# Kernel optimization log

Measured on AMD Instinct MI355X. Metric: run time of the kernel, lower is better.

Reference implementation:

```python
import jax, jax.numpy as jnp
import numpy as np

B, S, D, H = 2, 2048, 1024, 16
HD = D // H  # head dim = 64


def setup_inputs() -> dict:
    key = jax.random.key(0)
    ks = jax.random.split(key, 5)
    scale = 1.0 / np.sqrt(D)
    return {
        "hidden_states": jax.random.normal(ks[0], (B, S, D), jnp.float32),
        "attention_mask": jax.random.normal(ks[1], (B, 1, 1, S), jnp.float32),
        "Wq": jax.random.normal(ks[2], (D, D), jnp.float32) * scale,
        "bq": jnp.zeros((D,), jnp.float32),
        "Wk": jax.random.normal(ks[3], (D, D), jnp.float32) * scale,
        "bk": jnp.zeros((D,), jnp.float32),
        "Wv": jax.random.normal(ks[4], (D, D), jnp.float32) * scale,
        "bv": jnp.zeros((D,), jnp.float32),
    }


def _split_heads(x):
    # [B,S,D] -> [B,H,S,HD]
    return x.reshape(B, S, H, HD).transpose(0, 2, 1, 3)


def reference(hidden_states, attention_mask, Wq, bq, Wk, bk, Wv, bv):
    # torch Linear: y = x @ W.T + b
    q = _split_heads(hidden_states @ Wq.T + bq)
    k = _split_heads(hidden_states @ Wk.T + bk)
    v = _split_heads(hidden_states @ Wv.T + bv)

    scores = jnp.einsum("bhqd,bhkd->bhqk", q, k)
    # Faithful to source: with a mask present, the 1/sqrt(head_dim) scaling
    # is overwritten and raw scores are multiplied by the binary key mask.
    mask = (attention_mask >= 0).astype(scores.dtype)  # [B,1,1,S]
    probs = scores * mask
    # dropout prob = 0 (eval) -> identity

    ctx = jnp.einsum("bhqk,bhkd->bhqd", probs, v)
    ctx = ctx.transpose(0, 2, 1, 3).reshape(B, S, D)
    return ctx
```

## Files before the change

### kernel.cpp

```cpp
#include <hip/hip_runtime.h>

#define BB 2
#define SS 2048
#define DD 1024
#define HH 16
#define HDIM 64
#define MTOT 4096

typedef unsigned short u16;
typedef __bf16 bf16_t;
typedef bf16_t bf16x8 __attribute__((ext_vector_type(8)));
typedef float floatx4 __attribute__((ext_vector_type(4)));
typedef float floatx16 __attribute__((ext_vector_type(16)));

__device__ __forceinline__ float bf2f(u16 u) {
  union { unsigned int i; float f; } x;
  x.i = ((unsigned int)u) << 16;
  return x.f;
}
__device__ __forceinline__ u16 f2bf(float f) {
  union { float f; unsigned int i; } x;
  x.f = f;
  unsigned int r = x.i + 0x7fffu + ((x.i >> 16) & 1u);
  return (u16)(r >> 16);
}

__device__ __forceinline__ void gload16(const u16* g, u16* l) {
  __builtin_amdgcn_global_load_lds(
      (const __attribute__((address_space(1))) unsigned int*)g,
      (__attribute__((address_space(3))) unsigned int*)l, 16, 0, 0);
}

__global__ __launch_bounds__(256) void cast_to_bf16(
    const float* __restrict__ hs, const float* __restrict__ wq,
    const float* __restrict__ wk, const float* __restrict__ wv,
    u16* __restrict__ hs_b, u16* __restrict__ wq_b,
    u16* __restrict__ wk_b, u16* __restrict__ wv_b) {
  int fid = blockIdx.x * 256 + threadIdx.x;
  const float* src;
  u16* dst;
  int local;
  if (fid < 1048576) { src = hs; dst = hs_b; local = fid; }
  else if (fid < 1310720) { src = wq; dst = wq_b; local = fid - 1048576; }
  else if (fid < 1572864) { src = wk; dst = wk_b; local = fid - 1310720; }
  else { src = wv; dst = wv_b; local = fid - 1572864; }
  float4 v = reinterpret_cast<const float4*>(src)[local];
  ushort4 o;
  o.x = f2bf(v.x); o.y = f2bf(v.y); o.z = f2bf(v.z); o.w = f2bf(v.w);
  reinterpret_cast<ushort4*>(dst)[local] = o;
}

#define BKK 32
__global__ __launch_bounds__(256) void qkv_gemm_kernel(
    const u16* __restrict__ A,
    const u16* __restrict__ Wq, const u16* __restrict__ Wk, const u16* __restrict__ Wv,
    const float* __restrict__ bq, const float* __restrict__ bk, const float* __restrict__ bv,
    u16* __restrict__ Qo, u16* __restrict__ Ko, u16* __restrict__ Vo) {
  __shared__ u16 sA[128 * BKK];
  __shared__ u16 sB[128 * BKK];
  const int mt = blockIdx.y, ntall = blockIdx.x;
  const int seg = ntall >> 3, nt = ntall & 7;
  const u16* Wp = (seg == 0) ? Wq : (seg == 1) ? Wk : Wv;
  const float* bp = (seg == 0) ? bq : (seg == 1) ? bk : bv;
  u16* Out = (seg == 0) ? Qo : (seg == 1) ? Ko : Vo;
  const int m0 = mt * 128, n0 = nt * 128;
  const int tid = threadIdx.x;
  const int lane = tid & 63, wave = tid >> 6;
  const int wm = (wave >> 1) * 64, wn = (wave & 1) * 64;
  const int l32 = lane & 31, khalf = lane >> 5;
  const int srow0 = wave * 32 + (lane >> 2);
  const int scol = (lane & 3) * 8;
  floatx16 acc[2][2] = {};
  for (int k0 = 0; k0 < DD; k0 += BKK) {
#pragma unroll
    for (int c = 0; c < 2; ++c) {
      int r = srow0 + c * 16;
      gload16(A + (size_t)(m0 + r) * DD + k0 + scol, sA + r * BKK + scol);
      gload16(Wp + (size_t)(n0 + r) * DD + k0 + scol, sB + r * BKK + scol);
    }
    __syncthreads();
#pragma unroll
    for (int kk = 0; kk < 2; ++kk) {
      bf16x8 af[2], bfr[2];
#pragma unroll
      for (int i = 0; i < 2; ++i)
        af[i] = *reinterpret_cast<const bf16x8*>(sA + (wm + i * 32 + l32) * BKK + kk * 16 + khalf * 8);
#pragma unroll
      for (int j = 0; j < 2; ++j)
        bfr[j] = *reinterpret_cast<const bf16x8*>(sB + (wn + j * 32 + l32) * BKK + kk * 16 + khalf * 8);
#pragma unroll
      for (int i = 0; i < 2; ++i)
#pragma unroll
        for (int j = 0; j < 2; ++j)
          acc[i][j] = __builtin_amdgcn_mfma_f32_32x32x16_bf16(af[i], bfr[j], acc[i][j], 0, 0, 0);
    }
    __syncthreads();
  }
#pragma unroll
  for (int j = 0; j < 2; ++j) {
    int col = n0 + wn + j * 32 + l32;
    float bias = bp[col];
#pragma unroll
    for (int i = 0; i < 2; ++i) {
#pragma unroll
      for (int reg = 0; reg < 16; ++reg) {
        int row = m0 + wm + i * 32 + (reg & 3) + 8 * (reg >> 2) + 4 * khalf;
        Out[(size_t)row * DD + col] = f2bf(acc[i][j][reg] + bias);
      }
    }
  }
}

__global__ __launch_bounds__(256) void m_partial_kernel(
    const u16* __restrict__ Kb, const u16* __restrict__ Vb,
    const float* __restrict__ am, float* __restrict__ mpart) {
  __shared__ float sK[64 * 68];
  __shared__ float sV[64 * 68];
  const int bh = blockIdx.y;
  const int b = bh >> 4, h = bh & 15;
  const int tid = threadIdx.x;
  const int e0 = (tid & 15) * 4, d0 = (tid >> 4) * 4;
  float acc[4][4] = {};
  for (int cs = 0; cs < 4; ++cs) {
    const int s0 = (blockIdx.x * 4 + cs) * 64;
    if (cs) __syncthreads();
#pragma unroll
    for (int c = 0; c < 2; ++c) {
      int L = tid + c * 256;
      int srow = L >> 3;
      int col = (L & 7) * 8;
      size_t g = (size_t)(b * SS + s0 + srow) * DD + h * HDIM + col;
      uint4 kraw = *reinterpret_cast<const uint4*>(Kb + g);
      uint4 vraw = *reinterpret_cast<const uint4*>(Vb + g);
      float m = (am[b * SS + s0 + srow] >= 0.f) ? 1.f : 0.f;
      unsigned int kw[4] = {kraw.x, kraw.y, kraw.z, kraw.w};
      unsigned int vw[4] = {vraw.x, vraw.y, vraw.z, vraw.w};
#pragma unroll
      for (int q = 0; q < 4; ++q) {
        sK[srow * 68 + col + 2 * q]     = m * bf2f((u16)(kw[q] & 0xffffu));
        sK[srow * 68 + col + 2 * q + 1] = m * bf2f((u16)(kw[q] >> 16));
        sV[srow * 68 + col + 2 * q]     = bf2f((u16)(vw[q] & 0xffffu));
        sV[srow * 68 + col + 2 * q + 1] = bf2f((u16)(vw[q] >> 16));
      }
    }
    __syncthreads();
    for (int s = 0; s < 64; ++s) {
      float4 kk = *reinterpret_cast<const float4*>(&sK[s * 68 + e0]);
      float4 vv = *reinterpret_cast<const float4*>(&sV[s * 68 + d0]);
      float ka[4] = {kk.x, kk.y, kk.z, kk.w};
      float va[4] = {vv.x, vv.y, vv.z, vv.w};
#pragma unroll
      for (int i = 0; i < 4; ++i)
#pragma unroll
        for (int j = 0; j < 4; ++j) acc[i][j] += ka[i] * va[j];
    }
  }
  float* outp = mpart + ((size_t)(blockIdx.x * 32 + bh)) * 4096;
#pragma unroll
  for (int i = 0; i < 4; ++i) {
    float4 o = {acc[i][0], acc[i][1], acc[i][2], acc[i][3]};
    *reinterpret_cast<float4*>(&outp[(e0 + i) * 64 + d0]) = o;
  }
}

__global__ __launch_bounds__(256) void ctx_kernel(
    const u16* __restrict__ Qb, const float* __restrict__ mpart, float* __restrict__ Out) {
  __shared__ float sM[64 * 68];
  __shared__ float sQ[64 * 68];
  const int mchunk = blockIdx.x;
  const int h = blockIdx.y;
  const int m0 = mchunk * 64;
  const int b = m0 >> 11;
  const int bh = b * HH + h;
  const int tid = threadIdx.x;
#pragma unroll
  for (int c = 0; c < 4; ++c) {
    int L4 = c * 256 + tid;
    float4 s = {0.f, 0.f, 0.f, 0.f};
#pragma unroll
    for (int pc = 0; pc < 8; ++pc) {
      const float4* p4 = reinterpret_cast<const float4*>(mpart + ((size_t)(pc * 32 + bh)) * 4096);
      float4 t = p4[L4];
      s.x += t.x; s.y += t.y; s.z += t.z; s.w += t.w;
    }
    int e = L4 >> 4, d = (L4 & 15) * 4;
    *reinterpret_cast<float4*>(&sM[e * 68 + d]) = s;
  }
#pragma unroll
  for (int c = 0; c < 2; ++c) {
    int L = tid + c * 256;
    int row = L >> 3, col = (L & 7) * 8;
    uint4 q = *reinterpret_cast<const uint4*>(Qb + (size_t)(m0 + row) * DD + h * HDIM + col);
    unsigned int w[4] = {q.x, q.y, q.z, q.w};
#pragma unroll
    for (int t = 0; t < 4; ++t) {
      sQ[row * 68 + col + 2 * t]     = bf2f((u16)(w[t] & 0xffffu));
      sQ[row * 68 + col + 2 * t + 1] = bf2f((u16)(w[t] >> 16));
    }
  }
  __syncthreads();
  const int d0 = (tid & 15) * 4, ml0 = (tid >> 4) * 4;
  float acc[4][4] = {};
  for (int e4 = 0; e4 < 64; e4 += 4) {
    float4 mm[4], qq[4];
#pragma unroll
    for (int t = 0; t < 4; ++t)
      mm[t] = *reinterpret_cast<const float4*>(&sM[(e4 + t) * 68 + d0]);
#pragma unroll
    for (int i = 0; i < 4; ++i)
      qq[i] = *reinterpret_cast<const float4*>(&sQ[(ml0 + i) * 68 + e4]);
    float ma[4][4], qa[4][4];
#pragma unroll
    for (int t = 0; t < 4; ++t) {
      ma[t][0] = mm[t].x; ma[t][1] = mm[t].y; ma[t][2] = mm[t].z; ma[t][3] = mm[t].w;
      qa[t][0] = qq[t].x; qa[t][1] = qq[t].y; qa[t][2] = qq[t].z; qa[t][3] = qq[t].w;
    }
#pragma unroll
    for (int i = 0; i < 4; ++i)
#pragma unroll
      for (int t = 0; t < 4; ++t)
#pragma unroll
        for (int j = 0; j < 4; ++j)
          acc[i][j] += qa[i][t] * ma[t][j];
  }
#pragma unroll
  for (int i = 0; i < 4; ++i) {
    float4 o = {acc[i][0], acc[i][1], acc[i][2], acc[i][3]};
    *reinterpret_cast<float4*>(Out + (size_t)(m0 + ml0 + i) * DD + h * HDIM + d0) = o;
  }
}

extern "C" void kernel_launch(void* const* d_in, const int* in_sizes, int n_in,
                              void* d_out, int out_size, void* d_ws, size_t ws_size,
                              hipStream_t stream) {
  const float* hs = (const float*)d_in[0];
  const float* am = (const float*)d_in[1];
  const float* wq = (const float*)d_in[2];
  const float* bq = (const float*)d_in[3];
  const float* wk = (const float*)d_in[4];
  const float* bk = (const float*)d_in[5];
  const float* wv = (const float*)d_in[6];
  const float* bv = (const float*)d_in[7];
  float* out = (float*)d_out;
  char* ws = (char*)d_ws;

  u16* hs_b = (u16*)(ws);
  u16* wq_b = (u16*)(ws + 8388608);
  u16* wk_b = (u16*)(ws + 10485760);
  u16* wv_b = (u16*)(ws + 12582912);
  u16* q_b  = (u16*)(ws + 14680064);
  u16* k_b  = (u16*)(ws + 23068672);
  u16* v_b  = (u16*)(ws + 31457280);
  float* mpart = (float*)(ws + 39845888);

  cast_to_bf16<<<7168, 256, 0, stream>>>(hs, wq, wk, wv, hs_b, wq_b, wk_b, wv_b);
  qkv_gemm_kernel<<<dim3(24, 32), 256, 0, stream>>>(hs_b, wq_b, wk_b, wv_b,
                                                    bq, bk, bv, q_b, k_b, v_b);
  m_partial_kernel<<<dim3(8, 32), 256, 0, stream>>>(k_b, v_b, am, mpart);
  ctx_kernel<<<dim3(64, 16), 256, 0, stream>>>(q_b, mpart, out);
}
```

Before: 158.3 us.

## Split M partial sums wider, add bf16 reduce kernel, use MFMA for ctx

After: 147.5 us. 1.07x faster.

```diff
diff --git a/kernel.cpp b/kernel.cpp
--- a/kernel.cpp
+++ b/kernel.cpp
@@ -112,48 +112,45 @@
 }
 
 __global__ __launch_bounds__(256) void m_partial_kernel(
-    const u16* __restrict__ Kb, const u16* __restrict__ Vb,
+    const u16* __restrict__ Xb, const u16* __restrict__ Yb,
     const float* __restrict__ am, float* __restrict__ mpart) {
-  __shared__ float sK[64 * 68];
-  __shared__ float sV[64 * 68];
+  __shared__ float sX[64 * 68];
+  __shared__ float sY[64 * 68];
   const int bh = blockIdx.y;
   const int b = bh >> 4, h = bh & 15;
   const int tid = threadIdx.x;
   const int e0 = (tid & 15) * 4, d0 = (tid >> 4) * 4;
+  const int s0 = blockIdx.x * 64;
   float acc[4][4] = {};
-  for (int cs = 0; cs < 4; ++cs) {
-    const int s0 = (blockIdx.x * 4 + cs) * 64;
-    if (cs) __syncthreads();
-#pragma unroll
-    for (int c = 0; c < 2; ++c) {
-      int L = tid + c * 256;
-      int srow = L >> 3;
-      int col = (L & 7) * 8;
-      size_t g = (size_t)(b * SS + s0 + srow) * DD + h * HDIM + col;
-      uint4 kraw = *reinterpret_cast<const uint4*>(Kb + g);
-      uint4 vraw = *reinterpret_cast<const uint4*>(Vb + g);
-      float m = (am[b * SS + s0 + srow] >= 0.f) ? 1.f : 0.f;
-      unsigned int kw[4] = {kraw.x, kraw.y, kraw.z, kraw.w};
-      unsigned int vw[4] = {vraw.x, vraw.y, vraw.z, vraw.w};
-#pragma unroll
-      for (int q = 0; q < 4; ++q) {
-        sK[srow * 68 + col + 2 * q]     = m * bf2f((u16)(kw[q] & 0xffffu));
-        sK[srow * 68 + col + 2 * q + 1] = m * bf2f((u16)(kw[q] >> 16));
-        sV[srow * 68 + col + 2 * q]     = bf2f((u16)(vw[q] & 0xffffu));
-        sV[srow * 68 + col + 2 * q + 1] = bf2f((u16)(vw[q] >> 16));
-      }
-    }
-    __syncthreads();
-    for (int s = 0; s < 64; ++s) {
-      float4 kk = *reinterpret_cast<const float4*>(&sK[s * 68 + e0]);
-      float4 vv = *reinterpret_cast<const float4*>(&sV[s * 68 + d0]);
-      float ka[4] = {kk.x, kk.y, kk.z, kk.w};
-      float va[4] = {vv.x, vv.y, vv.z, vv.w};
-#pragma unroll
-      for (int i = 0; i < 4; ++i)
-#pragma unroll
-        for (int j = 0; j < 4; ++j) acc[i][j] += ka[i] * va[j];
-    }
+#pragma unroll
+  for (int c = 0; c < 2; ++c) {
+    int L = tid + c * 256;
+    int srow = L >> 3;
+    int col = (L & 7) * 8;
+    size_t g = (size_t)(b * SS + s0 + srow) * DD + h * HDIM + col;
+    uint4 xraw = *reinterpret_cast<const uint4*>(Xb + g);
+    uint4 yraw = *reinterpret_cast<const uint4*>(Yb + g);
+    float m = (am[b * SS + s0 + srow] >= 0.f) ? 1.f : 0.f;
+    unsigned int xw[4] = {xraw.x, xraw.y, xraw.z, xraw.w};
+    unsigned int yw[4] = {yraw.x, yraw.y, yraw.z, yraw.w};
+#pragma unroll
+    for (int q = 0; q < 4; ++q) {
+      sX[srow * 68 + col + 2 * q]     = m * bf2f((u16)(xw[q] & 0xffffu));
+      sX[srow * 68 + col + 2 * q + 1] = m * bf2f((u16)(xw[q] >> 16));
+      sY[srow * 68 + col + 2 * q]     = bf2f((u16)(yw[q] & 0xffffu));
+      sY[srow * 68 + col + 2 * q + 1] = bf2f((u16)(yw[q] >> 16));
+    }
+  }
+  __syncthreads();
+  for (int s = 0; s < 64; ++s) {
+    float4 xx = *reinterpret_cast<const float4*>(&sX[s * 68 + e0]);
+    float4 yy = *reinterpret_cast<const float4*>(&sY[s * 68 + d0]);
+    float xa[4] = {xx.x, xx.y, xx.z, xx.w};
+    float ya[4] = {yy.x, yy.y, yy.z, yy.w};
+#pragma unroll
+    for (int i = 0; i < 4; ++i)
+#pragma unroll
+      for (int j = 0; j < 4; ++j) acc[i][j] += xa[i] * ya[j];
   }
   float* outp = mpart + ((size_t)(blockIdx.x * 32 + bh)) * 4096;
 #pragma unroll
@@ -163,70 +160,64 @@
   }
 }
 
+__global__ __launch_bounds__(128) void m_reduce_kernel(
+    const float* __restrict__ mpart, u16* __restrict__ Mb) {
+  int t = blockIdx.x * 128 + threadIdx.x;
+  const float* p = mpart + (size_t)t * 4;
+  float4 s = {0.f, 0.f, 0.f, 0.f};
+#pragma unroll
+  for (int pc = 0; pc < 32; ++pc) {
+    float4 v = *reinterpret_cast<const float4*>(p + (size_t)pc * 131072);
+    s.x += v.x; s.y += v.y; s.z += v.z; s.w += v.w;
+  }
+  ushort4 o = {f2bf(s.x), f2bf(s.y), f2bf(s.z), f2bf(s.w)};
+  *reinterpret_cast<ushort4*>(Mb + (size_t)t * 4) = o;
+}
+
 __global__ __launch_bounds__(256) void ctx_kernel(
-    const u16* __restrict__ Qb, const float* __restrict__ mpart, float* __restrict__ Out) {
-  __shared__ float sM[64 * 68];
-  __shared__ float sQ[64 * 68];
-  const int mchunk = blockIdx.x;
+    const u16* __restrict__ Qb, const u16* __restrict__ Mb, float* __restrict__ Out) {
+  __shared__ u16 sMT[64 * 72];
+  const int m0 = blockIdx.x * 128;
   const int h = blockIdx.y;
-  const int m0 = mchunk * 64;
   const int b = m0 >> 11;
   const int bh = b * HH + h;
   const int tid = threadIdx.x;
-#pragma unroll
-  for (int c = 0; c < 4; ++c) {
-    int L4 = c * 256 + tid;
-    float4 s = {0.f, 0.f, 0.f, 0.f};
-#pragma unroll
-    for (int pc = 0; pc < 8; ++pc) {
-      const float4* p4 = reinterpret_cast<const float4*>(mpart + ((size_t)(pc * 32 + bh)) * 4096);
-      float4 t = p4[L4];
-      s.x += t.x; s.y += t.y; s.z += t.z; s.w += t.w;
-    }
-    int e = L4 >> 4, d = (L4 & 15) * 4;
-    *reinterpret_cast<float4*>(&sM[e * 68 + d]) = s;
-  }
+  const u16* mg = Mb + (size_t)bh * 4096;
 #pragma unroll
   for (int c = 0; c < 2; ++c) {
-    int L = tid + c * 256;
-    int row = L >> 3, col = (L & 7) * 8;
-    uint4 q = *reinterpret_cast<const uint4*>(Qb + (size_t)(m0 + row) * DD + h * HDIM + col);
-    unsigned int w[4] = {q.x, q.y, q.z, q.w};
-#pragma unroll
-    for (int t = 0; t < 4; ++t) {
-      sQ[row * 68 + col + 2 * t]     = bf2f((u16)(w[t] & 0xffffu));
-      sQ[row * 68 + col + 2 * t + 1] = bf2f((u16)(w[t] >> 16));
-    }
+    int L = c * 256 + tid;
+    int d = L >> 3, e = (L & 7) * 8;
+    *reinterpret_cast<uint4*>(&sMT[d * 72 + e]) =
+        *reinterpret_cast<const uint4*>(&mg[d * 64 + e]);
   }
   __syncthreads();
-  const int d0 = (tid & 15) * 4, ml0 = (tid >> 4) * 4;
-  float acc[4][4] = {};
-  for (int e4 = 0; e4 < 64; e4 += 4) {
-    float4 mm[4], qq[4];
-#pragma unroll
-    for (int t = 0; t < 4; ++t)
-      mm[t] = *reinterpret_cast<const float4*>(&sM[(e4 + t) * 68 + d0]);
-#pragma unroll
-    for (int i = 0; i < 4; ++i)
-      qq[i] = *reinterpret_cast<const float4*>(&sQ[(ml0 + i) * 68 + e4]);
-    float ma[4][4], qa[4][4];
-#pragma unroll
-    for (int t = 0; t < 4; ++t) {
-      ma[t][0] = mm[t].x; ma[t][1] = mm[t].y; ma[t][2] = mm[t].z; ma[t][3] = mm[t].w;
-      qa[t][0] = qq[t].x; qa[t][1] = qq[t].y; qa[t][2] = qq[t].z; qa[t][3] = qq[t].w;
-    }
-#pragma unroll
-    for (int i = 0; i < 4; ++i)
-#pragma unroll
-      for (int t = 0; t < 4; ++t)
-#pragma unroll
-        for (int j = 0; j < 4; ++j)
-          acc[i][j] += qa[i][t] * ma[t][j];
-  }
-#pragma unroll
-  for (int i = 0; i < 4; ++i) {
-    float4 o = {acc[i][0], acc[i][1], acc[i][2], acc[i][3]};
-    *reinterpret_cast<float4*>(Out + (size_t)(m0 + ml0 + i) * DD + h * HDIM + d0) = o;
+  const int lane = tid & 63, wave = tid >> 6;
+  const int l32 = lane & 31, khalf = lane >> 5;
+  const int arow = m0 + wave * 32 + l32;
+  const u16* qrow = Qb + (size_t)arow * DD + h * HDIM + khalf * 8;
+  bf16x8 af[4], bfr[2][4];
+#pragma unroll
+  for (int k0 = 0; k0 < 4; ++k0) {
+    af[k0] = *reinterpret_cast<const bf16x8*>(qrow + k0 * 16);
+#pragma unroll
+    for (int j = 0; j < 2; ++j)
+      bfr[j][k0] = *reinterpret_cast<const bf16x8*>(
+          &sMT[(j * 32 + l32) * 72 + k0 * 16 + khalf * 8]);
+  }
+  floatx16 acc[2] = {};
+#pragma unroll
+  for (int j = 0; j < 2; ++j)
+#pragma unroll
+    for (int k0 = 0; k0 < 4; ++k0)
+      acc[j] = __builtin_amdgcn_mfma_f32_32x32x16_bf16(af[k0], bfr[j][k0], acc[j], 0, 0, 0);
+#pragma unroll
+  for (int j = 0; j < 2; ++j) {
+    int col = h * HDIM + j * 32 + l32;
+#pragma unroll
+    for (int reg = 0; reg < 16; ++reg) {
+      int r = m0 + wave * 32 + (reg & 3) + 8 * (reg >> 2) + 4 * khalf;
+      Out[(size_t)r * DD + col] = acc[j][reg];
+    }
   }
 }
 
@@ -252,10 +243,12 @@
   u16* k_b  = (u16*)(ws + 23068672);
   u16* v_b  = (u16*)(ws + 31457280);
   float* mpart = (float*)(ws + 39845888);
+  u16* m_b  = (u16*)(ws + 56623104);
 
   cast_to_bf16<<<7168, 256, 0, stream>>>(hs, wq, wk, wv, hs_b, wq_b, wk_b, wv_b);
   qkv_gemm_kernel<<<dim3(24, 32), 256, 0, stream>>>(hs_b, wq_b, wk_b, wv_b,
                                                     bq, bk, bv, q_b, k_b, v_b);
-  m_partial_kernel<<<dim3(8, 32), 256, 0, stream>>>(k_b, v_b, am, mpart);
-  ctx_kernel<<<dim3(64, 16), 256, 0, stream>>>(q_b, mpart, out);
-}
+  m_partial_kernel<<<dim3(32, 32), 256, 0, stream>>>(v_b, k_b, am, mpart);
+  m_reduce_kernel<<<256, 128, 0, stream>>>(mpart, m_b);
+  ctx_kernel<<<dim3(32, 16), 256, 0, stream>>>(q_b, m_b, out);
+}
```
